# Kernel optimization log

Hardware: AMD Instinct MI355X
Metric: run time of the kernel (lower is better)

Reference implementation:

```python
import jax, jax.numpy as jnp
import numpy as np

FIN = 4096
N_MEM = 256
SQRT_FIN = 64  # int(FIN ** 0.5)


def setup_inputs() -> dict:
    key = jax.random.key(0)
    ks = jax.random.split(key, 6)
    scale = 0.02  # keep relu-relu scores numerically tame
    x = jax.random.normal(ks[0], (1024, FIN), dtype=jnp.float32)
    Wq = jax.random.normal(ks[1], (FIN, SQRT_FIN * N_MEM), dtype=jnp.float32) * scale
    bq = jnp.zeros((SQRT_FIN * N_MEM,), dtype=jnp.float32)
    Wk = jax.random.normal(ks[2], (FIN, SQRT_FIN * N_MEM), dtype=jnp.float32) * scale
    bk = jnp.zeros((SQRT_FIN * N_MEM,), dtype=jnp.float32)
    v = jax.random.normal(ks[3], (N_MEM, FIN), dtype=jnp.float32) * scale
    Wl = jax.random.normal(ks[4], (FIN, FIN), dtype=jnp.float32) * scale
    bl = jnp.zeros((FIN,), dtype=jnp.float32)
    return {"x": x, "Wq": Wq, "bq": bq, "Wk": Wk, "bk": bk, "v": v, "Wl": Wl, "bl": bl}


def reference(x, Wq, bq, Wk, bk, v, Wl, bl):
    B = x.shape[0]
    # Q/K projections, reshaped to [B, n_mem, sqrt_fin]
    xq = (x @ Wq + bq).reshape(B, N_MEM, SQRT_FIN)
    xk = (x @ Wk + bk).reshape(B, N_MEM, SQRT_FIN)
    # relu-relu score matrix [B, n_mem, n_mem], scaled by sqrt(sqrt_fin)
    scores = jnp.einsum('bms,bns->bmn', jax.nn.relu(xq), jax.nn.relu(xk))
    scores = scores / jnp.sqrt(jnp.asarray(SQRT_FIN, dtype=x.dtype))
    # multiply by learned value memory v [n_mem, fin] (broadcast over batch)
    mem = jnp.einsum('bmn,nf->bmf', scores, v)
    # mean over memory slots, output projection, residual
    pooled = mem.mean(axis=1)  # [B, fin]
    return x + (pooled @ Wl + bl)
```

## Files before the change

### kernel.cpp

```cpp
#include <hip/hip_runtime.h>
#include <hip/hip_bf16.h>
#include <stdint.h>

#define B_SZ 1024
#define FIN  4096
#define NMEM 256
#define NQK  16384

typedef __attribute__((ext_vector_type(8))) short short8;
typedef __attribute__((ext_vector_type(4))) float floatx4;

__device__ __forceinline__ ushort f2bf(float f) {
    uint32_t u = __float_as_uint(f);
    return (ushort)((u + 0x7fffu + ((u >> 16) & 1u)) >> 16);
}
__device__ __forceinline__ float bf2f(ushort u) {
    return __uint_as_float(((uint32_t)u) << 16);
}

__device__ __forceinline__ void gl2lds16(const void* g, void* l) {
    __builtin_amdgcn_global_load_lds(
        (const __attribute__((address_space(1))) void*)g,
        (__attribute__((address_space(3))) void*)l, 16, 0, 0);
}

__global__ void cvt_kernel(const float* __restrict__ src, ushort* __restrict__ dst, int n) {
    int i = (blockIdx.x * blockDim.x + threadIdx.x) * 8;
    if (i >= n) return;
    float4 f0 = *(const float4*)(src + i);
    float4 f1 = *(const float4*)(src + i + 4);
    uint4 o;
    o.x = (uint32_t)f2bf(f0.x) | ((uint32_t)f2bf(f0.y) << 16);
    o.y = (uint32_t)f2bf(f0.z) | ((uint32_t)f2bf(f0.w) << 16);
    o.z = (uint32_t)f2bf(f1.x) | ((uint32_t)f2bf(f1.y) << 16);
    o.w = (uint32_t)f2bf(f1.z) | ((uint32_t)f2bf(f1.w) << 16);
    *(uint4*)(dst + i) = o;
}

__global__ __launch_bounds__(256)
void transT_kernel(const float* __restrict__ src, ushort* __restrict__ dst,
                   int NFULL, int n0) {
    __shared__ float lds[64 * 65];
    const int tid = threadIdx.x;
    const int nc0 = blockIdx.x * 64;
    const int k0  = blockIdx.y * 64;
    #pragma unroll
    for (int p = 0; p < 4; ++p) {
        int idx = p * 256 + tid;
        int krow = idx >> 4;
        int c4 = (idx & 15) * 4;
        float4 v = *(const float4*)(src + (size_t)(k0 + krow) * NFULL + n0 + nc0 + c4);
        lds[krow * 65 + c4 + 0] = v.x;
        lds[krow * 65 + c4 + 1] = v.y;
        lds[krow * 65 + c4 + 2] = v.z;
        lds[krow * 65 + c4 + 3] = v.w;
    }
    __syncthreads();
    #pragma unroll
    for (int p = 0; p < 2; ++p) {
        int idx = p * 256 + tid;
        int nrow = idx >> 3;
        int c8 = (idx & 7) * 8;
        ushort t[8];
        #pragma unroll
        for (int j = 0; j < 8; ++j) t[j] = f2bf(lds[(c8 + j) * 65 + nrow]);
        uint4 o;
        o.x = (uint32_t)t[0] | ((uint32_t)t[1] << 16);
        o.y = (uint32_t)t[2] | ((uint32_t)t[3] << 16);
        o.z = (uint32_t)t[4] | ((uint32_t)t[5] << 16);
        o.w = (uint32_t)t[6] | ((uint32_t)t[7] << 16);
        *(uint4*)(dst + (size_t)(nc0 + nrow) * 4096 + k0 + c8) = o;
    }
}

template<int RELU, int HASBIAS, int RESID, int OUTBF>
__global__ __launch_bounds__(256)
void gemm_bf(const ushort* __restrict__ A, const ushort* __restrict__ Bt,
             const float* __restrict__ bias, const float* __restrict__ resid,
             void* __restrict__ Cout, int ldc, int M, int K)
{
    __shared__ __align__(16) ushort As[128 * 64];
    __shared__ __align__(16) ushort Bs[128 * 64];

    const int tid  = threadIdx.x;
    const int lane = tid & 63;
    const int wave = tid >> 6;
    const int wm = (wave >> 1) * 64;
    const int wn = (wave & 1) * 64;
    const int m0 = blockIdx.y * 128;
    const int n0 = blockIdx.x * 128;

    const int fr = lane & 15;
    const int fq = lane >> 4;

    floatx4 acc[4][4] = {};

    for (int k0 = 0; k0 < K; k0 += 64) {
        __syncthreads();
        #pragma unroll
        for (int i = 0; i < 4; ++i) {
            int id = i * 256 + wave * 64 + lane;
            int row = id >> 3, pos = id & 7;
            int c = pos ^ (row & 7);
            gl2lds16(A + (size_t)(m0 + row) * K + k0 + c * 8,
                     &As[(i * 256 + wave * 64) * 8]);
        }
        #pragma unroll
        for (int i = 0; i < 4; ++i) {
            int id = i * 256 + wave * 64 + lane;
            int row = id >> 3, pos = id & 7;
            int c = pos ^ (row & 7);
            gl2lds16(Bt + (size_t)(n0 + row) * K + k0 + c * 8,
                     &Bs[(i * 256 + wave * 64) * 8]);
        }
        __syncthreads();

        #pragma unroll
        for (int ks = 0; ks < 2; ++ks) {
            short8 a[4], b[4];
            #pragma unroll
            for (int i = 0; i < 4; ++i) {
                int row = wm + i * 16 + fr;
                int p = (ks * 4 + fq) ^ (row & 7);
                a[i] = *(const short8*)(&As[row * 64 + p * 8]);
            }
            #pragma unroll
            for (int i = 0; i < 4; ++i) {
                int row = wn + i * 16 + fr;
                int p = (ks * 4 + fq) ^ (row & 7);
                b[i] = *(const short8*)(&Bs[row * 64 + p * 8]);
            }
            #pragma unroll
            for (int mi = 0; mi < 4; ++mi)
                #pragma unroll
                for (int ni = 0; ni < 4; ++ni)
                    acc[mi][ni] = __builtin_amdgcn_mfma_f32_16x16x32_bf16(
                        a[mi], b[ni], acc[mi][ni], 0, 0, 0);
        }
    }

    #pragma unroll
    for (int mi = 0; mi < 4; ++mi) {
        #pragma unroll
        for (int ni = 0; ni < 4; ++ni) {
            #pragma unroll
            for (int r = 0; r < 4; ++r) {
                int gm = m0 + wm + mi * 16 + fq * 4 + r;
                int gn = n0 + wn + ni * 16 + fr;
                float val = acc[mi][ni][r];
                if (HASBIAS) val += bias[gn];
                if (RELU)    val = fmaxf(val, 0.0f);
                if (RESID)   val += resid[(size_t)gm * ldc + gn];
                if (OUTBF) ((ushort*)Cout)[(size_t)gm * ldc + gn] = f2bf(val);
                else       ((float*)Cout)[(size_t)gm * ldc + gn] = val;
            }
        }
    }
}

#define BM 128
#define BN 128
#define BKK 64
#define LDA 72
#define LDB 72

template<int RELU, int HASBIAS, int RESID, int OUTBF>
__global__ __launch_bounds__(256)
void gemm_k(const ushort* __restrict__ A, const float* __restrict__ B,
            const float* __restrict__ bias, const float* __restrict__ resid,
            void* __restrict__ Cout, int M, int N, int K)
{
    __shared__ ushort As[BM * LDA];
    __shared__ ushort Bs[BN * LDB];

    const int tid  = threadIdx.x;
    const int lane = tid & 63;
    const int wave = tid >> 6;
    const int wm = (wave >> 1) * 64;
    const int wn = (wave & 1) * 64;
    const int m0 = blockIdx.y * BM;
    const int n0 = blockIdx.x * BN;

    const int fr = lane & 15;
    const int fq = lane >> 4;

    floatx4 acc[4][4] = {};

    for (int k0 = 0; k0 < K; k0 += BKK) {
        __syncthreads();
        #pragma unroll
        for (int c = 0; c < 4; ++c) {
            int idx = c * 256 + tid;
            int row = idx >> 3;
            int off = idx & 7;
            *(uint4*)(&As[row * LDA + off * 8]) =
                *(const uint4*)(A + (size_t)(m0 + row) * K + k0 + off * 8);
        }
        #pragma unroll
        for (int p = 0; p < 8; ++p) {
            int idx = p * 256 + tid;
            int nn = idx & 127;
            int kg = idx >> 7;
            const float* bp = B + (size_t)(k0 + kg * 4) * N + n0 + nn;
            float f0 = bp[0];
            float f1 = bp[N];
            float f2 = bp[2 * (size_t)N];
            float f3 = bp[3 * (size_t)N];
            ushort4 w;
            w.x = f2bf(f0); w.y = f2bf(f1); w.z = f2bf(f2); w.w = f2bf(f3);
            *(ushort4*)(&Bs[nn * LDB + kg * 4]) = w;
        }
        __syncthreads();

        #pragma unroll
        for (int ks = 0; ks < 2; ++ks) {
            short8 a[4], b[4];
            #pragma unroll
            for (int i = 0; i < 4; ++i)
                a[i] = *(const short8*)(&As[(wm + i * 16 + fr) * LDA + ks * 32 + fq * 8]);
            #pragma unroll
            for (int i = 0; i < 4; ++i)
                b[i] = *(const short8*)(&Bs[(wn + i * 16 + fr) * LDB + ks * 32 + fq * 8]);
            #pragma unroll
            for (int mi = 0; mi < 4; ++mi)
                #pragma unroll
                for (int ni = 0; ni < 4; ++ni)
                    acc[mi][ni] = __builtin_amdgcn_mfma_f32_16x16x32_bf16(
                        a[mi], b[ni], acc[mi][ni], 0, 0, 0);
        }
    }

    #pragma unroll
    for (int mi = 0; mi < 4; ++mi) {
        #pragma unroll
        for (int ni = 0; ni < 4; ++ni) {
            #pragma unroll
            for (int r = 0; r < 4; ++r) {
                int gm = m0 + wm + mi * 16 + fq * 4 + r;
                int gn = n0 + wn + ni * 16 + fr;
                float val = acc[mi][ni][r];
                if (HASBIAS) val += bias[gn];
                if (RELU)    val = fmaxf(val, 0.0f);
                if (RESID)   val += resid[(size_t)gm * N + gn];
                if (OUTBF) ((ushort*)Cout)[(size_t)gm * N + gn] = f2bf(val);
                else       ((float*)Cout)[(size_t)gm * N + gn] = val;
            }
        }
    }
}

__global__ void qbar_kernel(const ushort* __restrict__ XQr, float* __restrict__ qbar) {
    int b = blockIdx.x;
    int s = threadIdx.x;
    const ushort* p = XQr + (size_t)b * NQK + s;
    float sum = 0.0f;
    #pragma unroll 4
    for (int m = 0; m < NMEM; ++m) sum += bf2f(p[m * 64]);
    qbar[b * 64 + s] = sum * (1.0f / (NMEM * 8.0f));
}

__global__ void spool_kernel(const ushort* __restrict__ XKr, const float* __restrict__ qbar,
                             ushort* __restrict__ spb) {
    int b = blockIdx.x;
    int n = threadIdx.x;
    __shared__ float q[64];
    if (threadIdx.x < 64) q[threadIdx.x] = qbar[b * 64 + threadIdx.x];
    __syncthreads();
    const ushort* p = XKr + (size_t)b * NQK + n * 64;
    float sum = 0.0f;
    #pragma unroll
    for (int s = 0; s < 64; s += 4) {
        ushort4 u = *(const ushort4*)(p + s);
        sum += bf2f(u.x) * q[s] + bf2f(u.y) * q[s + 1]
             + bf2f(u.z) * q[s + 2] + bf2f(u.w) * q[s + 3];
    }
    spb[b * 256 + n] = f2bf(sum);
}

extern "C" void kernel_launch(void* const* d_in, const int* in_sizes, int n_in,
                              void* d_out, int out_size, void* d_ws, size_t ws_size,
                              hipStream_t stream) {
    const float* x  = (const float*)d_in[0];
    const float* Wq = (const float*)d_in[1];
    const float* bq = (const float*)d_in[2];
    const float* Wk = (const float*)d_in[3];
    const float* bk = (const float*)d_in[4];
    const float* v  = (const float*)d_in[5];
    const float* Wl = (const float*)d_in[6];
    const float* bl = (const float*)d_in[7];
    float* out = (float*)d_out;

    const size_t MB = 1ull << 20;
    char* ws = (char*)d_ws;
    ushort* xb   = (ushort*)(ws + 0);
    ushort* XQr  = (ushort*)(ws + 8 * MB);
    ushort* XKr  = (ushort*)(ws + 40 * MB);
    float*  qbar = (float*)(ws + 72 * MB);
    ushort* spb  = (ushort*)(ws + 73 * MB);
    ushort* p2b  = (ushort*)(ws + 74 * MB);
    ushort* WT   = (ushort*)(ws + 82 * MB);

    cvt_kernel<<<dim3((B_SZ * FIN) / 8 / 256), 256, 0, stream>>>(x, xb, B_SZ * FIN);

    for (int c = 0; c < 2; ++c) {
        int n0 = c * 8192;
        transT_kernel<<<dim3(8192 / 64, FIN / 64), 256, 0, stream>>>(Wq, WT, NQK, n0);
        gemm_bf<1, 1, 0, 1><<<dim3(8192 / 128, B_SZ / 128), 256, 0, stream>>>(
            xb, WT, bq + n0, nullptr, XQr + n0, NQK, B_SZ, FIN);
    }
    qbar_kernel<<<dim3(B_SZ), 64, 0, stream>>>(XQr, qbar);

    for (int c = 0; c < 2; ++c) {
        int n0 = c * 8192;
        transT_kernel<<<dim3(8192 / 64, FIN / 64), 256, 0, stream>>>(Wk, WT, NQK, n0);
        gemm_bf<1, 1, 0, 1><<<dim3(8192 / 128, B_SZ / 128), 256, 0, stream>>>(
            xb, WT, bk + n0, nullptr, XKr + n0, NQK, B_SZ, FIN);
    }
    spool_kernel<<<dim3(B_SZ), 256, 0, stream>>>(XKr, qbar, spb);

    gemm_k<0, 0, 0, 1><<<dim3(FIN / BN, B_SZ / BM), 256, 0, stream>>>(
        spb, v, nullptr, nullptr, p2b, B_SZ, FIN, NMEM);

    transT_kernel<<<dim3(FIN / 64, FIN / 64), 256, 0, stream>>>(Wl, WT, FIN, 0);
    gemm_bf<0, 1, 1, 0><<<dim3(FIN / 128, B_SZ / 128), 256, 0, stream>>>(
        p2b, WT, bl, x, out, FIN, B_SZ, FIN);
}
```

Baseline: 1.028 ms.

## Add 256x256 double-buffered bf16 MFMA GEMM for Q/K projections

Adds a new 512-thread GEMM kernel with 256x256 output tiles, double-buffered LDS staged through direct global-to-LDS loads, XOR-swizzled layout and interleaved MFMA clusters with priority hints. It replaces the 128x128 GEMM for the two large Q/K projections and merges each pair of half-width launches into one full-width transpose plus GEMM. The larger tiles aim to raise operand reuse and overlap the loads with compute. The cost is higher register and LDS pressure, a grid of only 256 blocks, and hand-placed waitcnt/barrier scheduling that must be correct.

```diff
diff --git a/kernel.cpp b/kernel.cpp
--- a/kernel.cpp
+++ b/kernel.cpp
@@ -71,6 +71,166 @@
         o.w = (uint32_t)t[6] | ((uint32_t)t[7] << 16);
         *(uint4*)(dst + (size_t)(nc0 + nrow) * 4096 + k0 + c8) = o;
     }
+}
+
+template<int RELU, int HASBIAS>
+__global__ __launch_bounds__(512, 2)
+void gemm256(const ushort* __restrict__ A, const ushort* __restrict__ Bt,
+             const float* __restrict__ bias, ushort* __restrict__ C,
+             int ldc, int K)
+{
+    __shared__ __align__(16) ushort As[2][256 * 64];
+    __shared__ __align__(16) ushort Bs[2][256 * 64];
+
+    const int tid  = threadIdx.x;
+    const int lane = tid & 63;
+    const int wave = tid >> 6;
+    const int wr   = wave >> 2;
+    const int wc   = wave & 3;
+    const int m0 = blockIdx.y * 256;
+    const int n0 = blockIdx.x * 256;
+    const int fr = lane & 15;
+    const int fq = lane >> 4;
+    const int NT = K >> 6;
+
+    floatx4 acc[8][4] = {};
+    short8 a_[4][2];
+    short8 b0_[2][2];
+    short8 b1_[2][2];
+
+    auto stage_half = [&](const ushort* __restrict__ G, int grow0, ushort* L,
+                          int h, int k0) {
+        #pragma unroll
+        for (int i = 0; i < 2; ++i) {
+            int id  = i * 512 + tid;
+            int row = h * 128 + (id >> 3);
+            int pos = id & 7;
+            int cc  = pos ^ (row & 7);
+            gl2lds16(G + (size_t)(grow0 + row) * K + k0 + cc * 8,
+                     L + h * 8192 + (i * 512 + wave * 64) * 8);
+        }
+    };
+
+#define LOAD_A(QM)                                                             \
+    {                                                                          \
+        _Pragma("unroll")                                                      \
+        for (int j = 0; j < 4; ++j) {                                          \
+            int r = wr * 128 + ((QM) * 4 + j) * 16 + fr;                       \
+            _Pragma("unroll")                                                  \
+            for (int ks = 0; ks < 2; ++ks) {                                   \
+                int p = (ks * 4 + fq) ^ (r & 7);                               \
+                a_[j][ks] = *(const short8*)(&Acur[r * 64 + p * 8]);           \
+            }                                                                  \
+        }                                                                      \
+    }
+
+#define LOAD_B(QN, BB)                                                         \
+    {                                                                          \
+        _Pragma("unroll")                                                      \
+        for (int j = 0; j < 2; ++j) {                                          \
+            int r = wc * 64 + ((QN) * 2 + j) * 16 + fr;                        \
+            _Pragma("unroll")                                                  \
+            for (int ks = 0; ks < 2; ++ks) {                                   \
+                int p = (ks * 4 + fq) ^ (r & 7);                               \
+                BB[j][ks] = *(const short8*)(&Bcur[r * 64 + p * 8]);           \
+            }                                                                  \
+        }                                                                      \
+    }
+
+#define MFMA_CL(QM, QN, BB)                                                    \
+    __builtin_amdgcn_s_setprio(1);                                             \
+    _Pragma("unroll")                                                          \
+    for (int ks = 0; ks < 2; ++ks)                                             \
+        _Pragma("unroll")                                                      \
+        for (int j = 0; j < 4; ++j)                                            \
+            _Pragma("unroll")                                                  \
+            for (int i = 0; i < 2; ++i)                                        \
+                acc[(QM) * 4 + j][(QN) * 2 + i] =                              \
+                    __builtin_amdgcn_mfma_f32_16x16x32_bf16(                   \
+                        a_[j][ks], BB[i][ks],                                  \
+                        acc[(QM) * 4 + j][(QN) * 2 + i], 0, 0, 0);             \
+    __builtin_amdgcn_s_setprio(0);
+
+    stage_half(A,  m0, &As[0][0], 0, 0);
+    stage_half(A,  m0, &As[0][0], 1, 0);
+    stage_half(Bt, n0, &Bs[0][0], 0, 0);
+    stage_half(Bt, n0, &Bs[0][0], 1, 0);
+
+    for (int kt = 0; kt < NT - 1; ++kt) {
+        const int cur = kt & 1;
+        const ushort* Acur = &As[cur][0];
+        const ushort* Bcur = &Bs[cur][0];
+        ushort* An = &As[cur ^ 1][0];
+        ushort* Bn = &Bs[cur ^ 1][0];
+        const int k0n = (kt + 1) << 6;
+
+        stage_half(A, m0, An, 0, k0n);
+        asm volatile("s_waitcnt vmcnt(2)" ::: "memory");
+        __builtin_amdgcn_s_barrier();
+        __builtin_amdgcn_sched_barrier(0);
+        LOAD_A(0);
+        LOAD_B(0, b0_);
+        asm volatile("s_waitcnt lgkmcnt(0)" ::: "memory");
+        __builtin_amdgcn_sched_barrier(0);
+        MFMA_CL(0, 0, b0_);
+        __builtin_amdgcn_s_barrier();
+
+        LOAD_B(1, b1_);
+        stage_half(A, m0, An, 1, k0n);
+        __builtin_amdgcn_s_barrier();
+        asm volatile("s_waitcnt lgkmcnt(0)" ::: "memory");
+        __builtin_amdgcn_sched_barrier(0);
+        MFMA_CL(0, 1, b1_);
+        __builtin_amdgcn_s_barrier();
+
+        LOAD_A(1);
+        stage_half(Bt, n0, Bn, 0, k0n);
+        __builtin_amdgcn_s_barrier();
+        asm volatile("s_waitcnt lgkmcnt(0)" ::: "memory");
+        __builtin_amdgcn_sched_barrier(0);
+        MFMA_CL(1, 0, b0_);
+        __builtin_amdgcn_s_barrier();
+
+        stage_half(Bt, n0, Bn, 1, k0n);
+        __builtin_amdgcn_s_barrier();
+        MFMA_CL(1, 1, b1_);
+        __builtin_amdgcn_s_barrier();
+    }
+
+    {
+        const ushort* Acur = &As[(NT - 1) & 1][0];
+        const ushort* Bcur = &Bs[(NT - 1) & 1][0];
+        asm volatile("s_waitcnt vmcnt(0)" ::: "memory");
+        __builtin_amdgcn_s_barrier();
+        __builtin_amdgcn_sched_barrier(0);
+        LOAD_A(0);
+        LOAD_B(0, b0_);
+        LOAD_B(1, b1_);
+        MFMA_CL(0, 0, b0_);
+        MFMA_CL(0, 1, b1_);
+        LOAD_A(1);
+        MFMA_CL(1, 0, b0_);
+        MFMA_CL(1, 1, b1_);
+    }
+
+    #pragma unroll
+    for (int mi = 0; mi < 8; ++mi) {
+        #pragma unroll
+        for (int ni = 0; ni < 4; ++ni) {
+            #pragma unroll
+            for (int r = 0; r < 4; ++r) {
+                int gm = m0 + wr * 128 + mi * 16 + fq * 4 + r;
+                int gn = n0 + wc * 64 + ni * 16 + fr;
+                float val = acc[mi][ni][r];
+                if (HASBIAS) val += bias[gn];
+                if (RELU)    val = fmaxf(val, 0.0f);
+                C[(size_t)gm * ldc + gn] = f2bf(val);
+            }
+        }
+    }
+#undef LOAD_A
+#undef LOAD_B
+#undef MFMA_CL
 }
 
 template<int RELU, int HASBIAS, int RESID, int OUTBF>
@@ -302,20 +462,14 @@
 
     cvt_kernel<<<dim3((B_SZ * FIN) / 8 / 256), 256, 0, stream>>>(x, xb, B_SZ * FIN);
 
-    for (int c = 0; c < 2; ++c) {
-        int n0 = c * 8192;
-        transT_kernel<<<dim3(8192 / 64, FIN / 64), 256, 0, stream>>>(Wq, WT, NQK, n0);
-        gemm_bf<1, 1, 0, 1><<<dim3(8192 / 128, B_SZ / 128), 256, 0, stream>>>(
-            xb, WT, bq + n0, nullptr, XQr + n0, NQK, B_SZ, FIN);
-    }
+    transT_kernel<<<dim3(NQK / 64, FIN / 64), 256, 0, stream>>>(Wq, WT, NQK, 0);
+    gemm256<1, 1><<<dim3(NQK / 256, B_SZ / 256), 512, 0, stream>>>(
+        xb, WT, bq, XQr, NQK, FIN);
     qbar_kernel<<<dim3(B_SZ), 64, 0, stream>>>(XQr, qbar);
 
-    for (int c = 0; c < 2; ++c) {
-        int n0 = c * 8192;
-        transT_kernel<<<dim3(8192 / 64, FIN / 64), 256, 0, stream>>>(Wk, WT, NQK, n0);
-        gemm_bf<1, 1, 0, 1><<<dim3(8192 / 128, B_SZ / 128), 256, 0, stream>>>(
-            xb, WT, bk + n0, nullptr, XKr + n0, NQK, B_SZ, FIN);
-    }
+    transT_kernel<<<dim3(NQK / 64, FIN / 64), 256, 0, stream>>>(Wk, WT, NQK, 0);
+    gemm256<1, 1><<<dim3(NQK / 256, B_SZ / 256), 512, 0, stream>>>(
+        xb, WT, bk, XKr, NQK, FIN);
     spool_kernel<<<dim3(B_SZ), 256, 0, stream>>>(XKr, qbar, spb);
 
     gemm_k<0, 0, 0, 1><<<dim3(FIN / BN, B_SZ / BM), 256, 0, stream>>>(
```

After: 1.049 ms. 1.02x slower.
